# Optimization experiments

Hardware: AMD Instinct MI355X
Metric: run time of the kernel (lower is better)

The kernel has to match this reference:

```python
import jax, jax.numpy as jnp
import numpy as np

BN_EPS = 1e-5
HIDDEN = 64
NUM_LAYERS = 8


def setup_inputs() -> dict:
    key = jax.random.key(0)
    ks = jax.random.split(key, 24)
    N, E, G = 100000, 1600000, 500
    H, L = HIDDEN, NUM_LAYERS
    rn = lambda k, s, sc=0.1: jax.random.normal(k, s, jnp.float32) * sc
    un = lambda k, s: jax.random.uniform(k, s, jnp.float32, 0.5, 1.5)
    inp = {}
    inp["x"] = jax.random.normal(ks[0], (N, 1), jnp.float32)
    inp["edge_index"] = jax.random.randint(ks[1], (2, E), 0, N, jnp.int32)
    inp["batch"] = jnp.sort(jax.random.randint(ks[2], (N,), 0, G, jnp.int32))
    inp["num_graphs"] = G
    inp["eps"] = rn(ks[3], (L,))
    inp["W1_first"] = rn(ks[4], (1, H))
    inp["W1_rest"] = rn(ks[5], (L - 1, H, H))
    inp["b1"] = rn(ks[6], (L, H))
    inp["g1"] = un(ks[7], (L, H))
    inp["be1"] = rn(ks[8], (L, H))
    inp["m1"] = rn(ks[9], (L, H))
    inp["v1"] = un(ks[10], (L, H))
    inp["W2"] = rn(ks[11], (L, H, H))
    inp["b2"] = rn(ks[12], (L, H))
    inp["g2"] = un(ks[13], (L, H))
    inp["be2"] = rn(ks[14], (L, H))
    inp["m2"] = rn(ks[15], (L, H))
    inp["v2"] = un(ks[16], (L, H))
    inp["lin1_w"] = rn(ks[17], (L * H, H), 0.05)
    inp["lin1_b"] = rn(ks[18], (H,))
    inp["lin2_w"] = rn(ks[19], (H, 3))
    inp["lin2_b"] = rn(ks[20], (3,))
    return inp


def _bn(h, g, b, m, v):
    # BatchNorm1d in eval mode: affine normalize with running stats
    return (h - m) * jax.lax.rsqrt(v + BN_EPS) * g + b


def reference(x, edge_index, batch, num_graphs, eps, W1_first, W1_rest, b1, g1,
              be1, m1, v1, W2, b2, g2, be2, m2, v2, lin1_w, lin1_b, lin2_w, lin2_b):
    src, dst = edge_index[0], edge_index[1]
    N = x.shape[0]
    h = x
    xs = []
    for i in range(NUM_LAYERS):
        # GINConv: scatter-add neighbor aggregation + (1+eps)*self, then MLP
        agg = jax.ops.segment_sum(h[src], dst, num_segments=N)  # [N, H_in]
        z = (1.0 + eps[i]) * h + agg
        W1 = W1_first if i == 0 else W1_rest[i - 1]
        z = jnp.maximum(z @ W1 + b1[i], 0.0)
        z = _bn(z, g1[i], be1[i], m1[i], v1[i])
        z = jnp.maximum(z @ W2[i] + b2[i], 0.0)
        z = _bn(z, g2[i], be2[i], m2[i], v2[i])
        h = z
        xs.append(h)
    jk = jnp.concatenate(xs, axis=-1)  # [N, L*H] JumpingKnowledge 'cat'
    sums = jax.ops.segment_sum(jk, batch, num_segments=num_graphs)
    counts = jax.ops.segment_sum(jnp.ones((N,), jk.dtype), batch, num_segments=num_graphs)
    pooled = sums / jnp.maximum(counts, 1.0)[:, None]  # global_mean_pool
    h = jnp.maximum(pooled @ lin1_w + lin1_b, 0.0)
    # dropout is identity in eval mode
    logits = h @ lin2_w + lin2_b
    return jax.nn.log_softmax(logits, axis=-1)
```

## Files before the change

kernel.cpp:

```cpp
#include <hip/hip_runtime.h>
#include <hip/hip_bf16.h>
#include <math.h>


typedef unsigned int uint;
typedef unsigned short ushort;
typedef __attribute__((ext_vector_type(8))) short short8;
typedef __attribute__((ext_vector_type(4))) float floatx4;
typedef __attribute__((ext_vector_type(4))) uint uintx4;

#define BBITS 10
#define BCAP 20480
#define BMASK ((1 << BBITS) - 1)

__device__ __forceinline__ float bf_lo(uint w) { return __uint_as_float(w << 16); }
__device__ __forceinline__ float bf_hi(uint w) { return __uint_as_float(w & 0xffff0000u); }

__device__ __forceinline__ ushort f2bf(float x) {
  __hip_bfloat16 h = __float2bfloat16(x);
  return *(ushort*)&h;
}
__device__ __forceinline__ float bf2f(ushort u) { return __uint_as_float((uint)u << 16); }

__device__ __forceinline__ uint pack_bf16(float a, float b) {
  return (uint)f2bf(a) | ((uint)f2bf(b) << 16);
}

__device__ __forceinline__ void split8(float4 u0, float4 u1, short8& hi, short8& lo) {
  float v0 = u0.x, v1 = u0.y, v2 = u0.z, v3 = u0.w;
  float v4 = u1.x, v5 = u1.y, v6 = u1.z, v7 = u1.w;
  ushort h0 = f2bf(v0), h1 = f2bf(v1), h2 = f2bf(v2), h3 = f2bf(v3);
  ushort h4 = f2bf(v4), h5 = f2bf(v5), h6 = f2bf(v6), h7 = f2bf(v7);
  hi[0] = (short)h0; hi[1] = (short)h1; hi[2] = (short)h2; hi[3] = (short)h3;
  hi[4] = (short)h4; hi[5] = (short)h5; hi[6] = (short)h6; hi[7] = (short)h7;
  lo[0] = (short)f2bf(v0 - bf2f(h0)); lo[1] = (short)f2bf(v1 - bf2f(h1));
  lo[2] = (short)f2bf(v2 - bf2f(h2)); lo[3] = (short)f2bf(v3 - bf2f(h3));
  lo[4] = (short)f2bf(v4 - bf2f(h4)); lo[5] = (short)f2bf(v5 - bf2f(h5));
  lo[6] = (short)f2bf(v6 - bf2f(h6)); lo[7] = (short)f2bf(v7 - bf2f(h7));
}


__global__ void init_bc_kernel(int* __restrict__ bc, int NB) {
  int b = threadIdx.x;
  if (b < NB) bc[b * 16] = b * BCAP;
}

__global__ __launch_bounds__(1024) void bin_edges_kernel(
    const int* __restrict__ src, const int* __restrict__ dst, int* __restrict__ bc,
    uint* __restrict__ arena, int E) {
  __shared__ int cnt[128], base[128];
  for (long chunk = (long)blockIdx.x * 4096; chunk < E; chunk += (long)gridDim.x * 4096) {
    if (threadIdx.x < 128) cnt[threadIdx.x] = 0;
    __syncthreads();
    uint v[4];
    int b[4], r[4];
#pragma unroll
    for (int u = 0; u < 4; ++u) {
      long e = chunk + threadIdx.x + u * 1024;
      if (e < E) {
        int s = src[e];
        int d = dst[e];
        b[u] = d >> BBITS;
        v[u] = ((uint)s << BBITS) | (uint)(d & BMASK);
        r[u] = atomicAdd(&cnt[b[u]], 1);
      }
    }
    __syncthreads();
    if (threadIdx.x < 128)
      base[threadIdx.x] = cnt[threadIdx.x] ? atomicAdd(&bc[threadIdx.x * 16], cnt[threadIdx.x]) : 0;
    __syncthreads();
#pragma unroll
    for (int u = 0; u < 4; ++u) {
      long e = chunk + threadIdx.x + u * 1024;
      if (e < E) arena[base[b[u]] + r[u]] = v[u];
    }
    __syncthreads();
  }
}

__global__ __launch_bounds__(1024) void bucket_count_kernel(
    const uint* __restrict__ arena, const int* __restrict__ bc,
    int* __restrict__ deg, int N) {
  __shared__ int hist[1 << BBITS];
  int b = blockIdx.x;
  int lo = b << BBITS;
  int hi = min(lo + (1 << BBITS), N);
  hist[threadIdx.x] = 0;
  __syncthreads();
  int cnt = bc[b * 16] - b * BCAP;
  const uint* ad = arena + (size_t)b * BCAP;
  for (int i = threadIdx.x; i < cnt; i += 1024) atomicAdd(&hist[ad[i] & BMASK], 1);
  __syncthreads();
  if (lo + (int)threadIdx.x < hi) deg[lo + threadIdx.x] = hist[threadIdx.x];
}

__global__ __launch_bounds__(1024) void bucket_scatter_kernel(
    const uint* __restrict__ arena, const int* __restrict__ bc,
    const int* __restrict__ rp, int* __restrict__ col, int N) {
  __shared__ int cur[1 << BBITS];
  int b = blockIdx.x;
  int lo = b << BBITS;
  int hi = min(lo + (1 << BBITS), N);
  if (lo + (int)threadIdx.x < hi) cur[threadIdx.x] = rp[lo + threadIdx.x];
  __syncthreads();
  int cnt = bc[b * 16] - b * BCAP;
  const uint* ad = arena + (size_t)b * BCAP;
  for (int i = threadIdx.x; i < cnt; i += 1024) {
    uint v = ad[i];
    int pos = atomicAdd(&cur[v & BMASK], 1);
    col[pos] = (int)(v >> BBITS);
  }
}

__global__ void scan_blocksums(const int* __restrict__ deg, int* __restrict__ bsum, int N) {
  __shared__ int red[256];
  int i = blockIdx.x * 256 + threadIdx.x;
  red[threadIdx.x] = (i < N) ? deg[i] : 0;
  __syncthreads();
  for (int off = 128; off > 0; off >>= 1) {
    if (threadIdx.x < off) red[threadIdx.x] += red[threadIdx.x + off];
    __syncthreads();
  }
  if (threadIdx.x == 0) bsum[blockIdx.x] = red[0];
}

__global__ void scan_bsum(const int* __restrict__ bsum, int* __restrict__ boff,
                          int* __restrict__ rp_last, int B) {
  __shared__ int tmp[1024];
  int t = threadIdx.x;
  int v = (t < B) ? bsum[t] : 0;
  tmp[t] = v;
  __syncthreads();
  for (int off = 1; off < 1024; off <<= 1) {
    int u = (t >= off) ? tmp[t - off] : 0;
    __syncthreads();
    tmp[t] += u;
    __syncthreads();
  }
  if (t < B) boff[t] = tmp[t] - v;
  if (t == 1023) *rp_last = tmp[1023];
}

__global__ void scan_final(const int* __restrict__ deg, const int* __restrict__ boff,
                           int* __restrict__ rp, int N) {
  __shared__ int tmp[256];
  int i = blockIdx.x * 256 + threadIdx.x;
  int v = (i < N) ? deg[i] : 0;
  tmp[threadIdx.x] = v;
  __syncthreads();
  for (int off = 1; off < 256; off <<= 1) {
    int u = (threadIdx.x >= off) ? tmp[threadIdx.x - off] : 0;
    __syncthreads();
    tmp[threadIdx.x] += u;
    __syncthreads();
  }
  if (i < N) rp[i] = boff[blockIdx.x] + tmp[threadIdx.x] - v;
}

__global__ void graph_bounds_kernel(const int* __restrict__ batch, int* __restrict__ gs,
                                    int N, int G) {
  int n = blockIdx.x * 256 + threadIdx.x;
  if (n >= N) return;
  int b = batch[n];
  int bp = (n == 0) ? -1 : batch[n - 1];
  for (int g = bp + 1; g <= b; ++g) gs[g] = n;
  if (n == N - 1)
    for (int g = b + 1; g <= G; ++g) gs[g] = N;
}

__global__ void prepack_w_kernel(const float* __restrict__ W1_rest,
                                 const float* __restrict__ W2, ushort* __restrict__ wp) {
  int l = blockIdx.x >> 1, g = blockIdx.x & 1;
  const float* W;
  if (g == 0) {
    if (l == 0) return;
    W = W1_rest + (size_t)(l - 1) * 4096;
  } else {
    W = W2 + (size_t)l * 4096;
  }
  ushort* out = wp + (size_t)(l * 2 + g) * 8192;
  for (int idx = threadIdx.x; idx < 4096; idx += blockDim.x) {
    int j = idx & 7, lane = (idx >> 3) & 63, ks = (idx >> 9) & 1, nt = (idx >> 10) & 3;
    int k = ks * 32 + (lane >> 4) * 8 + j;
    int n = nt * 16 + (lane & 15);
    float w = W[k * 64 + n];
    ushort hi = f2bf(w);
    ushort lo = f2bf(w - bf2f(hi));
    size_t base = (size_t)((nt * 2 + ks) * 2) * 512 + lane * 8 + j;
    out[base] = hi;
    out[base + 512] = lo;
  }
}

__global__ __launch_bounds__(256, 8) void agg_kernel(
    const ushort* __restrict__ hb, const int* __restrict__ rp,
    const int* __restrict__ col, const float* __restrict__ eps,
    int layer, ushort* __restrict__ zb, int N) {
  int lane = threadIdx.x & 63;
  int g = lane >> 3;
  int r = lane & 7;
  int wave = blockIdx.x * (blockDim.x >> 6) + (threadIdx.x >> 6);
  int nwaves = gridDim.x * (blockDim.x >> 6);
  float ep = 1.0f + eps[layer];
  for (int n = wave * 2; n < N; n += nwaves * 2) {
    int n0 = __builtin_amdgcn_readfirstlane(n);
    int n1 = n0 + 1;
    int beg0 = rp[n0];
    int end0 = rp[n0 + 1];
    int end1 = (n1 < N) ? rp[n1 + 1] : end0;
    float a0[8] = {0.f, 0.f, 0.f, 0.f, 0.f, 0.f, 0.f, 0.f};
    float a1[8] = {0.f, 0.f, 0.f, 0.f, 0.f, 0.f, 0.f, 0.f};
    float b0[8] = {0.f, 0.f, 0.f, 0.f, 0.f, 0.f, 0.f, 0.f};
    float b1v[8] = {0.f, 0.f, 0.f, 0.f, 0.f, 0.f, 0.f, 0.f};
    int e0 = beg0 + g;
    int e1 = end0 + g;
    while (e0 < end0 || e1 < end1) {
      if (e0 < end0) {
        int s = col[e0];
        uint4 w = ((const uint4*)(hb + (long)s * 64))[r];
        a0[0] += bf_lo(w.x); a0[1] += bf_hi(w.x);
        a0[2] += bf_lo(w.y); a0[3] += bf_hi(w.y);
        a0[4] += bf_lo(w.z); a0[5] += bf_hi(w.z);
        a0[6] += bf_lo(w.w); a0[7] += bf_hi(w.w);
      }
      if (e0 + 8 < end0) {
        int s = col[e0 + 8];
        uint4 w = ((const uint4*)(hb + (long)s * 64))[r];
        a1[0] += bf_lo(w.x); a1[1] += bf_hi(w.x);
        a1[2] += bf_lo(w.y); a1[3] += bf_hi(w.y);
        a1[4] += bf_lo(w.z); a1[5] += bf_hi(w.z);
        a1[6] += bf_lo(w.w); a1[7] += bf_hi(w.w);
      }
      if (e1 < end1) {
        int s = col[e1];
        uint4 w = ((const uint4*)(hb + (long)s * 64))[r];
        b0[0] += bf_lo(w.x); b0[1] += bf_hi(w.x);
        b0[2] += bf_lo(w.y); b0[3] += bf_hi(w.y);
        b0[4] += bf_lo(w.z); b0[5] += bf_hi(w.z);
        b0[6] += bf_lo(w.w); b0[7] += bf_hi(w.w);
      }
      if (e1 + 8 < end1) {
        int s = col[e1 + 8];
        uint4 w = ((const uint4*)(hb + (long)s * 64))[r];
        b1v[0] += bf_lo(w.x); b1v[1] += bf_hi(w.x);
        b1v[2] += bf_lo(w.y); b1v[3] += bf_hi(w.y);
        b1v[4] += bf_lo(w.z); b1v[5] += bf_hi(w.z);
        b1v[6] += bf_lo(w.w); b1v[7] += bf_hi(w.w);
      }
      e0 += 16; e1 += 16;
    }
#pragma unroll
    for (int j = 0; j < 8; ++j) { a0[j] += a1[j]; b0[j] += b1v[j]; }
#pragma unroll
    for (int m = 8; m <= 32; m <<= 1) {
#pragma unroll
      for (int j = 0; j < 8; ++j) {
        a0[j] += __shfl_xor(a0[j], m, 64);
        b0[j] += __shfl_xor(b0[j], m, 64);
      }
    }
    if (g == 0) {
      uint4 hv = ((const uint4*)(hb + (long)n0 * 64))[r];
      float v0 = fmaf(ep, bf_lo(hv.x), a0[0]), v1 = fmaf(ep, bf_hi(hv.x), a0[1]);
      float v2 = fmaf(ep, bf_lo(hv.y), a0[2]), v3 = fmaf(ep, bf_hi(hv.y), a0[3]);
      float v4 = fmaf(ep, bf_lo(hv.z), a0[4]), v5 = fmaf(ep, bf_hi(hv.z), a0[5]);
      float v6 = fmaf(ep, bf_lo(hv.w), a0[6]), v7 = fmaf(ep, bf_hi(hv.w), a0[7]);
      uintx4 w;
      w.x = pack_bf16(v0, v1); w.y = pack_bf16(v2, v3);
      w.z = pack_bf16(v4, v5); w.w = pack_bf16(v6, v7);
      __builtin_nontemporal_store(w, (uintx4*)(zb + (size_t)n0 * 64 + r * 8));
    } else if (g == 1 && n1 < N) {
      uint4 hv = ((const uint4*)(hb + (long)n1 * 64))[r];
      float v0 = fmaf(ep, bf_lo(hv.x), b0[0]), v1 = fmaf(ep, bf_hi(hv.x), b0[1]);
      float v2 = fmaf(ep, bf_lo(hv.y), b0[2]), v3 = fmaf(ep, bf_hi(hv.y), b0[3]);
      float v4 = fmaf(ep, bf_lo(hv.z), b0[4]), v5 = fmaf(ep, bf_hi(hv.z), b0[5]);
      float v6 = fmaf(ep, bf_lo(hv.w), b0[6]), v7 = fmaf(ep, bf_hi(hv.w), b0[7]);
      uintx4 w;
      w.x = pack_bf16(v0, v1); w.y = pack_bf16(v2, v3);
      w.z = pack_bf16(v4, v5); w.w = pack_bf16(v6, v7);
      __builtin_nontemporal_store(w, (uintx4*)(zb + (size_t)n1 * 64 + r * 8));
    }
  }
}

__global__ __launch_bounds__(256) void mfma_mlp_kernel(
    const ushort* __restrict__ zb, const float* __restrict__ z0,
    const float* __restrict__ W1f, ushort* __restrict__ hout,
    const ushort* __restrict__ wp1, const ushort* __restrict__ wp2,
    const float* __restrict__ b1, const float* __restrict__ g1,
    const float* __restrict__ be1, const float* __restrict__ m1,
    const float* __restrict__ v1,
    const float* __restrict__ b2, const float* __restrict__ g2,
    const float* __restrict__ be2, const float* __restrict__ m2,
    const float* __restrict__ v2,
    const int* __restrict__ batch, float* __restrict__ pooled,
    int layer, int skip1, int N) {
  __shared__ float bnp[6][64];
  __shared__ float w1fl[64];
  __shared__ float sbuf[64][68];
  __shared__ int batchl[64];
  int tid = threadIdx.x;
  int blockbase = blockIdx.x * 64;
  if (tid < 64) {
    bnp[0][tid] = b1[tid];
    float s1 = g1[tid] * rsqrtf(v1[tid] + 1e-5f);
    bnp[1][tid] = s1;
    bnp[2][tid] = be1[tid] - m1[tid] * s1;
    bnp[3][tid] = b2[tid];
    float s2 = g2[tid] * rsqrtf(v2[tid] + 1e-5f);
    bnp[4][tid] = s2;
    bnp[5][tid] = be2[tid] - m2[tid] * s2;
    batchl[tid] = (blockbase + tid < N) ? batch[blockbase + tid] : -1;
    if (skip1) w1fl[tid] = W1f[tid];
  }
  __syncthreads();
  int wave = tid >> 6, lane = tid & 63;
  int q = lane >> 4, c = lane & 15;
  int base = blockbase + wave * 16;

  short8 ahi0, alo0, ahi1, alo1;
  if (!skip1) {
    {
      long row = base + c;
      if (row >= N) row = N - 1;
      const ushort* zr = zb + row * 64;
      ahi0 = __builtin_nontemporal_load((const short8*)(zr + q * 8));
      ahi1 = __builtin_nontemporal_load((const short8*)(zr + 32 + q * 8));
    }
    floatx4 acc[4];
#pragma unroll
    for (int nt = 0; nt < 4; ++nt) acc[nt] = (floatx4){0.f, 0.f, 0.f, 0.f};
#pragma unroll
    for (int nt = 0; nt < 4; ++nt) {
#pragma unroll
      for (int ks = 0; ks < 2; ++ks) {
        const ushort* fb = wp1 + ((nt * 2 + ks) * 2) * 512 + lane * 8;
        short8 bh = *(const short8*)fb;
        short8 bl = *(const short8*)(fb + 512);
        short8 ah = ks ? ahi1 : ahi0;
        acc[nt] = __builtin_amdgcn_mfma_f32_16x16x32_bf16(ah, bh, acc[nt], 0, 0, 0);
        acc[nt] = __builtin_amdgcn_mfma_f32_16x16x32_bf16(ah, bl, acc[nt], 0, 0, 0);
      }
    }
#pragma unroll
    for (int nt = 0; nt < 4; ++nt) {
      int feat = nt * 16 + c;
      float s1 = bnp[1][feat], o1 = bnp[2][feat], bb = bnp[0][feat];
#pragma unroll
      for (int r = 0; r < 4; ++r) {
        float y = fmaxf(acc[nt][r] + bb, 0.f);
        sbuf[wave * 16 + q * 4 + r][feat] = fmaf(y, s1, o1);
      }
    }
    float4 u0 = *(const float4*)&sbuf[wave * 16 + c][q * 8];
    float4 u1 = *(const float4*)&sbuf[wave * 16 + c][q * 8 + 4];
    split8(u0, u1, ahi0, alo0);
    u0 = *(const float4*)&sbuf[wave * 16 + c][32 + q * 8];
    u1 = *(const float4*)&sbuf[wave * 16 + c][32 + q * 8 + 4];
    split8(u0, u1, ahi1, alo1);
  } else {
    long row = base + c;
    if (row >= N) row = N - 1;
    float zv = z0[row];
    float4 t00, t01, t10, t11;
    {
      float tv[8];
#pragma unroll
      for (int j = 0; j < 8; ++j) {
        int k = q * 8 + j;
        float y = fmaxf(fmaf(zv, w1fl[k], bnp[0][k]), 0.f);
        tv[j] = fmaf(y, bnp[1][k], bnp[2][k]);
      }
      t00 = make_float4(tv[0], tv[1], tv[2], tv[3]);
      t01 = make_float4(tv[4], tv[5], tv[6], tv[7]);
#pragma unroll
      for (int j = 0; j < 8; ++j) {
        int k = 32 + q * 8 + j;
        float y = fmaxf(fmaf(zv, w1fl[k], bnp[0][k]), 0.f);
        tv[j] = fmaf(y, bnp[1][k], bnp[2][k]);
      }
      t10 = make_float4(tv[0], tv[1], tv[2], tv[3]);
      t11 = make_float4(tv[4], tv[5], tv[6], tv[7]);
    }
    split8(t00, t01, ahi0, alo0);
    split8(t10, t11, ahi1, alo1);
  }

  floatx4 acc2[4];
#pragma unroll
  for (int nt = 0; nt < 4; ++nt) acc2[nt] = (floatx4){0.f, 0.f, 0.f, 0.f};
#pragma unroll
  for (int nt = 0; nt < 4; ++nt) {
#pragma unroll
    for (int ks = 0; ks < 2; ++ks) {
      const ushort* fb = wp2 + ((nt * 2 + ks) * 2) * 512 + lane * 8;
      short8 bh = *(const short8*)fb;
      short8 bl = *(const short8*)(fb + 512);
      short8 ah = ks ? ahi1 : ahi0;
      short8 al = ks ? alo1 : alo0;
      acc2[nt] = __builtin_amdgcn_mfma_f32_16x16x32_bf16(ah, bh, acc2[nt], 0, 0, 0);
      acc2[nt] = __builtin_amdgcn_mfma_f32_16x16x32_bf16(al, bh, acc2[nt], 0, 0, 0);
      acc2[nt] = __builtin_amdgcn_mfma_f32_16x16x32_bf16(ah, bl, acc2[nt], 0, 0, 0);
    }
  }

#pragma unroll
  for (int nt = 0; nt < 4; ++nt) {
    int feat = nt * 16 + c;
    float s2 = bnp[4][feat], o2 = bnp[5][feat], bb = bnp[3][feat];
#pragma unroll
    for (int r = 0; r < 4; ++r) {
      int node = base + q * 4 + r;
      int li = wave * 16 + q * 4 + r;
      float val = 0.f;
      if (node < N) {
        float y = fmaxf(acc2[nt][r] + bb, 0.f);
        val = fmaf(y, s2, o2);
        hout[(long)node * 64 + feat] = f2bf(val);
      }
      sbuf[li][feat] = val;
    }
  }
  __syncthreads();

  if (tid < 64) {
    int j = tid;
    int nvalid = N - blockbase;
    if (nvalid > 64) nvalid = 64;
    int i = 0;
    while (i < nvalid) {
      int g = batchl[i];
      float s = 0.f;
      while (i < nvalid && batchl[i] == g) { s += sbuf[i][j]; ++i; }
      atomicAdd(&pooled[(size_t)g * 512 + layer * 64 + j], s);
    }
  }
}

__global__ void z0_kernel(const float* __restrict__ x, const int* __restrict__ rp,
                          const int* __restrict__ col, const float* __restrict__ eps,
                          float* __restrict__ z0, int N) {
  int n = blockIdx.x * blockDim.x + threadIdx.x;
  if (n >= N) return;
  int beg = rp[n], end = rp[n + 1];
  float a = 0.f;
  for (int e = beg; e < end; ++e) a += x[col[e]];
  z0[n] = fmaf(1.0f + eps[0], x[n], a);
}

__global__ __launch_bounds__(64) void final_kernel(
    const float* __restrict__ pooled, const int* __restrict__ gs,
    const float* __restrict__ lin1_w, const float* __restrict__ lin1_b,
    const float* __restrict__ lin2_w, const float* __restrict__ lin2_b,
    float* __restrict__ out, int G) {
  int g = blockIdx.x;
  int j = threadIdx.x;
  float inv = 1.0f / fmaxf((float)(gs[g + 1] - gs[g]), 1.0f);
  __shared__ float p[512];
  for (int t = j; t < 512; t += 64) p[t] = pooled[(long)g * 512 + t] * inv;
  __syncthreads();
  float a0 = lin1_b[j], a1 = 0.f, a2 = 0.f, a3 = 0.f;
  for (int k = 0; k < 512; k += 4) {
    a0 = fmaf(p[k + 0], lin1_w[(k + 0) * 64 + j], a0);
    a1 = fmaf(p[k + 1], lin1_w[(k + 1) * 64 + j], a1);
    a2 = fmaf(p[k + 2], lin1_w[(k + 2) * 64 + j], a2);
    a3 = fmaf(p[k + 3], lin1_w[(k + 3) * 64 + j], a3);
  }
  float hv = fmaxf((a0 + a1) + (a2 + a3), 0.f);
  __shared__ float hb[64];
  hb[j] = hv;
  __syncthreads();
  __shared__ float lg[3];
  if (j < 3) {
    float a = lin2_b[j];
#pragma unroll
    for (int k = 0; k < 64; ++k) a = fmaf(hb[k], lin2_w[k * 3 + j], a);
    lg[j] = a;
  }
  __syncthreads();
  if (j < 3) {
    float mx = fmaxf(fmaxf(lg[0], lg[1]), lg[2]);
    float lse = mx + logf(expf(lg[0] - mx) + expf(lg[1] - mx) + expf(lg[2] - mx));
    out[g * 3 + j] = lg[j] - lse;
  }
}

extern "C" void kernel_launch(void* const* d_in, const int* in_sizes, int n_in,
                              void* d_out, int out_size, void* d_ws, size_t ws_size,
                              hipStream_t stream) {
  const float* x        = (const float*)d_in[0];
  const int*   edge     = (const int*)d_in[1];
  const int*   batch    = (const int*)d_in[2];
  const float* eps      = (const float*)d_in[4];
  const float* W1_first = (const float*)d_in[5];
  const float* W1_rest  = (const float*)d_in[6];
  const float* b1       = (const float*)d_in[7];
  const float* g1       = (const float*)d_in[8];
  const float* be1      = (const float*)d_in[9];
  const float* m1       = (const float*)d_in[10];
  const float* v1       = (const float*)d_in[11];
  const float* W2       = (const float*)d_in[12];
  const float* b2       = (const float*)d_in[13];
  const float* g2       = (const float*)d_in[14];
  const float* be2      = (const float*)d_in[15];
  const float* m2       = (const float*)d_in[16];
  const float* v2       = (const float*)d_in[17];
  const float* lin1_w   = (const float*)d_in[18];
  const float* lin1_b   = (const float*)d_in[19];
  const float* lin2_w   = (const float*)d_in[20];
  const float* lin2_b   = (const float*)d_in[21];

  int N = in_sizes[0];
  int E = in_sizes[1] / 2;
  int G = out_size / 3;
  const int* esrc = edge;
  const int* edst = edge + E;
  int NB = (N + (1 << BBITS) - 1) >> BBITS;
  if (NB > 128) NB = 128;

  size_t off = 0;
  auto alloc = [&](size_t bytes) -> char* {
    char* p = (char*)d_ws + off;
    off += (bytes + 255) & ~(size_t)255;
    return p;
  };
  int SB = (N + 255) / 256;
  int*    deg    = (int*)alloc((size_t)N * 4);
  int*    rp     = (int*)alloc((size_t)(N + 1) * 4);
  int*    col    = (int*)alloc((size_t)E * 4);
  int*    bsum   = (int*)alloc((size_t)SB * 4);
  int*    boff   = (int*)alloc((size_t)SB * 4);
  int*    bc     = (int*)alloc((size_t)128 * 16 * 4);
  uint*   arena  = (uint*)alloc((size_t)NB * BCAP * 4);
  int*    gs     = (int*)alloc((size_t)(G + 1) * 4);
  ushort* wpack  = (ushort*)alloc((size_t)16 * 8192 * 2);
  float*  z0buf  = (float*)alloc((size_t)N * 4);
  ushort* zbuf   = (ushort*)alloc((size_t)N * 64 * 2);
  ushort* hA     = (ushort*)alloc((size_t)N * 64 * 2);
  ushort* hB     = (ushort*)alloc((size_t)N * 64 * 2);
  float*  pooled = (float*)alloc((size_t)G * 512 * 4);
  (void)ws_size;

  init_bc_kernel<<<1, 128, 0, stream>>>(bc, NB);
  int ebA = (E + 4095) / 4096;
  bin_edges_kernel<<<ebA, 1024, 0, stream>>>(esrc, edst, bc, arena, E);
  bucket_count_kernel<<<NB, 1024, 0, stream>>>(arena, bc, deg, N);
  scan_blocksums<<<SB, 256, 0, stream>>>(deg, bsum, N);
  scan_bsum<<<1, 1024, 0, stream>>>(bsum, boff, rp + N, SB);
  scan_final<<<SB, 256, 0, stream>>>(deg, boff, rp, N);
  bucket_scatter_kernel<<<NB, 1024, 0, stream>>>(arena, bc, rp, col, N);

  graph_bounds_kernel<<<SB, 256, 0, stream>>>(batch, gs, N, G);
  prepack_w_kernel<<<16, 256, 0, stream>>>(W1_rest, W2, wpack);
  (void)hipMemsetAsync(pooled, 0, (size_t)G * 512 * 4, stream);

  int nb = (N + 63) / 64;
  z0_kernel<<<SB, 256, 0, stream>>>(x, rp, col, eps, z0buf, N);
  mfma_mlp_kernel<<<nb, 256, 0, stream>>>(zbuf, z0buf, W1_first, hA,
      wpack, wpack + 8192,
      b1, g1, be1, m1, v1, b2, g2, be2, m2, v2, batch, pooled, 0, 1, N);

  ushort* hin = hA;
  ushort* hout = hB;
  for (int i = 1; i < 8; ++i) {
    agg_kernel<<<2048, 256, 0, stream>>>(hin, rp, col, eps, i, zbuf, N);
    mfma_mlp_kernel<<<nb, 256, 0, stream>>>(zbuf, z0buf, W1_first, hout,
        wpack + (size_t)(2 * i) * 8192, wpack + (size_t)(2 * i + 1) * 8192,
        b1 + i * 64, g1 + i * 64, be1 + i * 64, m1 + i * 64, v1 + i * 64,
        b2 + i * 64, g2 + i * 64, be2 + i * 64, m2 + i * 64, v2 + i * 64,
        batch, pooled, i, 0, N);
    ushort* t = hin; hin = hout; hout = t;
  }
  final_kernel<<<G, 64, 0, stream>>>(pooled, gs, lin1_w, lin1_b,
                                     lin2_w, lin2_b, (float*)d_out, G);
}
```

Baseline: 641.2 us.

## Enlarge MLP blocks to 128 nodes, coalesce bf16 output stores, parallelize pooling

```diff
diff --git a/kernel.cpp b/kernel.cpp
--- a/kernel.cpp
+++ b/kernel.cpp
@@ -283,7 +283,7 @@
   }
 }
 
-__global__ __launch_bounds__(256) void mfma_mlp_kernel(
+__global__ __launch_bounds__(512) void mfma_mlp_kernel(
     const ushort* __restrict__ zb, const float* __restrict__ z0,
     const float* __restrict__ W1f, ushort* __restrict__ hout,
     const ushort* __restrict__ wp1, const ushort* __restrict__ wp2,
@@ -297,10 +297,10 @@
     int layer, int skip1, int N) {
   __shared__ float bnp[6][64];
   __shared__ float w1fl[64];
-  __shared__ float sbuf[64][68];
-  __shared__ int batchl[64];
+  __shared__ float sbuf[128][68];
+  __shared__ int batchl[128];
   int tid = threadIdx.x;
-  int blockbase = blockIdx.x * 64;
+  int blockbase = blockIdx.x * 128;
   if (tid < 64) {
     bnp[0][tid] = b1[tid];
     float s1 = g1[tid] * rsqrtf(v1[tid] + 1e-5f);
@@ -310,13 +310,14 @@
     float s2 = g2[tid] * rsqrtf(v2[tid] + 1e-5f);
     bnp[4][tid] = s2;
     bnp[5][tid] = be2[tid] - m2[tid] * s2;
-    batchl[tid] = (blockbase + tid < N) ? batch[blockbase + tid] : -1;
     if (skip1) w1fl[tid] = W1f[tid];
   }
+  if (tid < 128) batchl[tid] = (blockbase + tid < N) ? batch[blockbase + tid] : -1;
   __syncthreads();
   int wave = tid >> 6, lane = tid & 63;
   int q = lane >> 4, c = lane & 15;
   int base = blockbase + wave * 16;
+  int srow = wave * 16;
 
   short8 ahi0, alo0, ahi1, alo1;
   if (!skip1) {
@@ -349,14 +350,14 @@
 #pragma unroll
       for (int r = 0; r < 4; ++r) {
         float y = fmaxf(acc[nt][r] + bb, 0.f);
-        sbuf[wave * 16 + q * 4 + r][feat] = fmaf(y, s1, o1);
-      }
-    }
-    float4 u0 = *(const float4*)&sbuf[wave * 16 + c][q * 8];
-    float4 u1 = *(const float4*)&sbuf[wave * 16 + c][q * 8 + 4];
+        sbuf[srow + q * 4 + r][feat] = fmaf(y, s1, o1);
+      }
+    }
+    float4 u0 = *(const float4*)&sbuf[srow + c][q * 8];
+    float4 u1 = *(const float4*)&sbuf[srow + c][q * 8 + 4];
     split8(u0, u1, ahi0, alo0);
-    u0 = *(const float4*)&sbuf[wave * 16 + c][32 + q * 8];
-    u1 = *(const float4*)&sbuf[wave * 16 + c][32 + q * 8 + 4];
+    u0 = *(const float4*)&sbuf[srow + c][32 + q * 8];
+    u1 = *(const float4*)&sbuf[srow + c][32 + q * 8 + 4];
     split8(u0, u1, ahi1, alo1);
   } else {
     long row = base + c;
@@ -411,27 +412,44 @@
 #pragma unroll
     for (int r = 0; r < 4; ++r) {
       int node = base + q * 4 + r;
-      int li = wave * 16 + q * 4 + r;
       float val = 0.f;
       if (node < N) {
         float y = fmaxf(acc2[nt][r] + bb, 0.f);
         val = fmaf(y, s2, o2);
-        hout[(long)node * 64 + feat] = f2bf(val);
-      }
-      sbuf[li][feat] = val;
-    }
-  }
-  __syncthreads();
-
-  if (tid < 64) {
-    int j = tid;
+      }
+      sbuf[srow + q * 4 + r][feat] = val;
+    }
+  }
+  __syncthreads();
+
+#pragma unroll
+  for (int it = 0; it < 2; ++it) {
+    int chunk = tid + it * 512;
+    int row = chunk >> 3, c8 = chunk & 7;
+    int node = blockbase + row;
+    if (node < N) {
+      const float* sp = &sbuf[row][c8 * 8];
+      uintx4 w;
+      w.x = pack_bf16(sp[0], sp[1]);
+      w.y = pack_bf16(sp[2], sp[3]);
+      w.z = pack_bf16(sp[4], sp[5]);
+      w.w = pack_bf16(sp[6], sp[7]);
+      *(uintx4*)(hout + (long)node * 64 + c8 * 8) = w;
+    }
+  }
+
+  if (tid < 256) {
+    int j = tid & 63;
+    int quarter = tid >> 6;
     int nvalid = N - blockbase;
-    if (nvalid > 64) nvalid = 64;
-    int i = 0;
-    while (i < nvalid) {
+    if (nvalid > 128) nvalid = 128;
+    int i = quarter * 32;
+    int iend = i + 32;
+    if (iend > nvalid) iend = nvalid;
+    while (i < iend) {
       int g = batchl[i];
       float s = 0.f;
-      while (i < nvalid && batchl[i] == g) { s += sbuf[i][j]; ++i; }
+      while (i < iend && batchl[i] == g) { s += sbuf[i][j]; ++i; }
       atomicAdd(&pooled[(size_t)g * 512 + layer * 64 + j], s);
     }
   }
@@ -554,9 +572,9 @@
   prepack_w_kernel<<<16, 256, 0, stream>>>(W1_rest, W2, wpack);
   (void)hipMemsetAsync(pooled, 0, (size_t)G * 512 * 4, stream);
 
-  int nb = (N + 63) / 64;
+  int nb = (N + 127) / 128;
   z0_kernel<<<SB, 256, 0, stream>>>(x, rp, col, eps, z0buf, N);
-  mfma_mlp_kernel<<<nb, 256, 0, stream>>>(zbuf, z0buf, W1_first, hA,
+  mfma_mlp_kernel<<<nb, 512, 0, stream>>>(zbuf, z0buf, W1_first, hA,
       wpack, wpack + 8192,
       b1, g1, be1, m1, v1, b2, g2, be2, m2, v2, batch, pooled, 0, 1, N);
 
@@ -564,7 +582,7 @@
   ushort* hout = hB;
   for (int i = 1; i < 8; ++i) {
     agg_kernel<<<2048, 256, 0, stream>>>(hin, rp, col, eps, i, zbuf, N);
-    mfma_mlp_kernel<<<nb, 256, 0, stream>>>(zbuf, z0buf, W1_first, hout,
+    mfma_mlp_kernel<<<nb, 512, 0, stream>>>(zbuf, z0buf, W1_first, hout,
         wpack + (size_t)(2 * i) * 8192, wpack + (size_t)(2 * i + 1) * 8192,
         b1 + i * 64, g1 + i * 64, be1 + i * 64, m1 + i * 64, v1 + i * 64,
         b2 + i * 64, g2 + i * 64, be2 + i * 64, m2 + i * 64, v2 + i * 64,
```

Result: no change. 636.3 us (-0.8%).
